# Optimization experiments

Measured on AMD Instinct MI355X. Metric: run time of the kernel, lower is better.

Reference implementation:

```python
import jax, jax.numpy as jnp
import numpy as np

D_MODEL = 256
N_HEADS = 8
D_K = D_MODEL // N_HEADS
D_HID = D_MODEL // 2
LN_EPS = 1e-5


def setup_inputs() -> dict:
    key = jax.random.key(0)
    ks = jax.random.split(key, 16)
    B, ND, NT = 4, 512, 512
    s = 1.0 / np.sqrt(D_MODEL)
    inp = {
        'detections': jax.random.normal(ks[0], (B, ND, D_MODEL), jnp.float32),
        'tracks': jax.random.normal(ks[1], (B, NT, D_MODEL), jnp.float32),
        # attention projections, torch Linear convention: W [out, in], y = x W^T + b
        'w_q': jax.random.normal(ks[2], (D_MODEL, D_MODEL), jnp.float32) * s,
        'b_q': jnp.zeros((D_MODEL,), jnp.float32),
        'w_k': jax.random.normal(ks[3], (D_MODEL, D_MODEL), jnp.float32) * s,
        'b_k': jnp.zeros((D_MODEL,), jnp.float32),
        'w_v': jax.random.normal(ks[4], (D_MODEL, D_MODEL), jnp.float32) * s,
        'b_v': jnp.zeros((D_MODEL,), jnp.float32),
        'w_o': jax.random.normal(ks[5], (D_MODEL, D_MODEL), jnp.float32) * s,
        'b_o': jnp.zeros((D_MODEL,), jnp.float32),
        # LayerNorm
        'ln_g': jnp.ones((D_MODEL,), jnp.float32),
        'ln_b': jnp.zeros((D_MODEL,), jnp.float32),
        # association head MLP
        'w1': jax.random.normal(ks[6], (D_HID, D_MODEL), jnp.float32) * s,
        'b1': jnp.zeros((D_HID,), jnp.float32),
        'w2': jax.random.normal(ks[7], (1, D_HID), jnp.float32) * (1.0 / np.sqrt(D_HID)),
        'b2': jnp.zeros((1,), jnp.float32),
    }
    return inp


def _forward(detections, tracks, w_q, b_q, w_k, b_k, w_v, b_v, w_o, b_o,
             ln_g, ln_b, w1, b1, w2, b2):
    B, ND, D = detections.shape
    NT = tracks.shape[1]
    # cross-attention: query=detections, key=value=tracks
    Q = (detections @ w_q.T + b_q).reshape(B, ND, N_HEADS, D_K).transpose(0, 2, 1, 3)
    K = (tracks @ w_k.T + b_k).reshape(B, NT, N_HEADS, D_K).transpose(0, 2, 1, 3)
    V = (tracks @ w_v.T + b_v).reshape(B, NT, N_HEADS, D_K).transpose(0, 2, 1, 3)
    scores = jnp.einsum('bhqd,bhkd->bhqk', Q, K) / np.sqrt(D_K)
    attn = jax.nn.softmax(scores, axis=-1)
    ctx = jnp.einsum('bhqk,bhkd->bhqd', attn, V)  # [B,H,ND,D_K]
    ctx = ctx.transpose(0, 2, 1, 3).reshape(B, ND, D)
    attended = ctx @ w_o.T + b_o
    # residual + LayerNorm (dropout = identity in eval)
    x = detections + attended
    mu = jnp.mean(x, axis=-1, keepdims=True)
    var = jnp.var(x, axis=-1, keepdims=True)
    xn = (x - mu) * jax.lax.rsqrt(var + LN_EPS) * ln_g + ln_b
    # pairwise broadcast-multiply + 2-layer MLP + sigmoid
    combined = xn[:, :, None, :] * tracks[:, None, :, :]  # [B,ND,NT,D]
    h = jax.nn.relu(jnp.einsum('bntd,hd->bnth', combined, w1) + b1)
    logits = jnp.einsum('bnth,oh->bnto', h, w2) + b2  # [B,ND,NT,1]
    return jax.nn.sigmoid(logits[..., 0])


def reference(detections, tracks, w_q, b_q, w_k, b_k, w_v, b_v, w_o, b_o,
              ln_g, ln_b, w1, b1, w2, b2):
    return _forward(detections, tracks, w_q, b_q, w_k, b_k, w_v, b_v, w_o, b_o,
                    ln_g, ln_b, w1, b1, w2, b2)
```

## Files before the change

### kernel.cpp

```cpp
#include <hip/hip_runtime.h>

typedef _Float16 half8 __attribute__((ext_vector_type(8)));
typedef _Float16 half4v __attribute__((ext_vector_type(4)));
typedef _Float16 half2v __attribute__((ext_vector_type(2)));
typedef float f32x4 __attribute__((ext_vector_type(4)));
typedef float f32x16 __attribute__((ext_vector_type(16)));

__device__ __forceinline__ half8 cvt8(const float4 a, const float4 b) {
    half8 r;
    r[0] = (_Float16)a.x; r[1] = (_Float16)a.y; r[2] = (_Float16)a.z; r[3] = (_Float16)a.w;
    r[4] = (_Float16)b.x; r[5] = (_Float16)b.y; r[6] = (_Float16)b.z; r[7] = (_Float16)b.w;
    return r;
}

__global__ __launch_bounds__(256) void qkv_kernel(
    const float* __restrict__ det, const float* __restrict__ trk,
    const float* __restrict__ wq, const float* __restrict__ wk,
    const float* __restrict__ wv, const float* __restrict__ bq,
    const float* __restrict__ bk, const float* __restrict__ bv,
    _Float16* __restrict__ Qh, _Float16* __restrict__ Kh,
    _Float16* __restrict__ vt)
{
    int z = blockIdx.z;
    const float* A    = (z == 0) ? det : trk;
    const float* Bm   = (z == 0) ? wq : (z == 1) ? wk : wv;
    const float* bias = (z == 0) ? bq : (z == 1) ? bk : bv;

    __shared__ _Float16 As[64][40];
    __shared__ _Float16 Bs[64][40];

    int tid = threadIdx.x, l = tid & 63, w = tid >> 6;
    int wm = (w >> 1) * 32, wn = (w & 1) * 32;
    int m0 = blockIdx.x * 64, n0 = blockIdx.y * 64;
    int lr = tid >> 2, lc = (tid & 3) * 8;
    int ko = (l >> 4) * 8, l15 = l & 15;

    f32x4 acc[2][2]{};

    for (int k0 = 0; k0 < 256; k0 += 32) {
        float4 a0 = *(const float4*)(A + (long)(m0 + lr) * 256 + k0 + lc);
        float4 a1 = *(const float4*)(A + (long)(m0 + lr) * 256 + k0 + lc + 4);
        float4 b0 = *(const float4*)(Bm + (long)(n0 + lr) * 256 + k0 + lc);
        float4 b1 = *(const float4*)(Bm + (long)(n0 + lr) * 256 + k0 + lc + 4);
        __syncthreads();
        *(half8*)&As[lr][lc] = cvt8(a0, a1);
        *(half8*)&Bs[lr][lc] = cvt8(b0, b1);
        __syncthreads();
        half8 af0 = *(const half8*)(&As[wm + l15][ko]);
        half8 af1 = *(const half8*)(&As[wm + 16 + l15][ko]);
        half8 bf0 = *(const half8*)(&Bs[wn + l15][ko]);
        half8 bf1 = *(const half8*)(&Bs[wn + 16 + l15][ko]);
        acc[0][0] = __builtin_amdgcn_mfma_f32_16x16x32_f16(af0, bf0, acc[0][0], 0, 0, 0);
        acc[0][1] = __builtin_amdgcn_mfma_f32_16x16x32_f16(af0, bf1, acc[0][1], 0, 0, 0);
        acc[1][0] = __builtin_amdgcn_mfma_f32_16x16x32_f16(af1, bf0, acc[1][0], 0, 0, 0);
        acc[1][1] = __builtin_amdgcn_mfma_f32_16x16x32_f16(af1, bf1, acc[1][1], 0, 0, 0);
    }

    #pragma unroll
    for (int mm = 0; mm < 2; ++mm)
    #pragma unroll
    for (int nn = 0; nn < 2; ++nn) {
        int row  = wm + mm * 16 + (l >> 4) * 4;
        int colg = n0 + wn + nn * 16 + l15;
        float bc = bias[colg];
        if (z == 2) {
            half4v hv;
            #pragma unroll
            for (int i = 0; i < 4; ++i) hv[i] = (_Float16)(acc[mm][nn][i] + bc);
            int grow = m0 + row;
            int bb = grow >> 9, t = grow & 511;
            long off = ((long)(bb * 8 + (colg >> 5)) * 32 + (colg & 31)) * 512 + t;
            *(half4v*)(vt + off) = hv;
        } else {
            _Float16* C = (z == 0) ? Qh : Kh;
            #pragma unroll
            for (int i = 0; i < 4; ++i)
                C[(long)(m0 + row + i) * 256 + colg] = (_Float16)(acc[mm][nn][i] + bc);
        }
    }
}

__global__ __launch_bounds__(256) void flash_kernel(
    const _Float16* __restrict__ Q, const _Float16* __restrict__ K,
    const _Float16* __restrict__ vt, _Float16* __restrict__ ctx)
{
    __shared__ _Float16 P[4][16][264];
    int bh = blockIdx.y, b = bh >> 3, h = bh & 7;
    int q0 = blockIdx.x * 64;
    int tid = threadIdx.x, l = tid & 63, w = tid >> 6;
    int l15 = l & 15, g = l >> 4;

    const _Float16* qp = Q + ((long)b * 512 + q0 + w * 16 + l15) * 256 + h * 32 + g * 8;
    half8 qf = *(const half8*)qp;
    #pragma unroll
    for (int i = 0; i < 8; ++i) qf[i] = qf[i] * (_Float16)0.17677669529663687f;

    const _Float16* kp = K + ((long)b * 512 + l15) * 256 + h * 32 + g * 8;
    const _Float16* vp = vt + ((long)bh * 32 + l15) * 512 + g * 8;

    f32x4 c0{}, c1{};
    float m_run = -3e38f, sum_run = 0.f;
    f32x4 zero{};

    #pragma unroll
    for (int hf = 0; hf < 2; ++hf) {
        f32x4 s[16];
        #pragma unroll
        for (int t = 0; t < 16; ++t) {
            half8 kf = *(const half8*)(kp + (long)(hf * 16 + t) * (16 * 256));
            s[t] = __builtin_amdgcn_mfma_f32_16x16x32_f16(kf, qf, zero, 0, 0, 0);
        }
        float m0 = -3e38f, m1 = -3e38f, m2 = -3e38f, m3 = -3e38f;
        #pragma unroll
        for (int t = 0; t < 16; ++t) {
            m0 = fmaxf(m0, s[t][0]); m1 = fmaxf(m1, s[t][1]);
            m2 = fmaxf(m2, s[t][2]); m3 = fmaxf(m3, s[t][3]);
        }
        float ml = fmaxf(fmaxf(m0, m1), fmaxf(m2, m3));
        ml = fmaxf(ml, __shfl_xor(ml, 16, 64));
        ml = fmaxf(ml, __shfl_xor(ml, 32, 64));
        float m_new = fmaxf(m_run, ml);
        float scale = __expf(m_run - m_new);
        #pragma unroll
        for (int i = 0; i < 4; ++i) { c0[i] *= scale; c1[i] *= scale; }
        sum_run *= scale;
        float s0 = 0.f, s1 = 0.f, s2 = 0.f, s3 = 0.f;
        #pragma unroll
        for (int t = 0; t < 16; ++t) {
            s[t][0] = __expf(s[t][0] - m_new); s0 += s[t][0];
            s[t][1] = __expf(s[t][1] - m_new); s1 += s[t][1];
            s[t][2] = __expf(s[t][2] - m_new); s2 += s[t][2];
            s[t][3] = __expf(s[t][3] - m_new); s3 += s[t][3];
        }
        sum_run += (s0 + s1) + (s2 + s3);
        m_run = m_new;

        #pragma unroll
        for (int t = 0; t < 16; ++t) {
            half2v p01, p23;
            p01[0] = (_Float16)s[t][0]; p01[1] = (_Float16)s[t][1];
            p23[0] = (_Float16)s[t][2]; p23[1] = (_Float16)s[t][3];
            *(half2v*)&P[w][l15][t * 16 + g * 4]     = p01;
            *(half2v*)&P[w][l15][t * 16 + g * 4 + 2] = p23;
        }
        #pragma unroll
        for (int s2i = 0; s2i < 8; ++s2i) {
            half8 bf = *(const half8*)&P[w][l15][s2i * 32 + g * 8];
            half8 a0 = *(const half8*)(vp + hf * 256 + s2i * 32);
            half8 a1 = *(const half8*)(vp + 16 * 512 + hf * 256 + s2i * 32);
            c0 = __builtin_amdgcn_mfma_f32_16x16x32_f16(a0, bf, c0, 0, 0, 0);
            c1 = __builtin_amdgcn_mfma_f32_16x16x32_f16(a1, bf, c1, 0, 0, 0);
        }
    }
    sum_run += __shfl_xor(sum_run, 16, 64);
    sum_run += __shfl_xor(sum_run, 32, 64);
    float rs = 1.f / sum_run;
    _Float16* cp = ctx + ((long)b * 512 + q0 + w * 16 + l15) * 256 + h * 32;
    #pragma unroll
    for (int i = 0; i < 4; ++i) {
        cp[g * 4 + i]      = (_Float16)(c0[i] * rs);
        cp[16 + g * 4 + i] = (_Float16)(c1[i] * rs);
    }
}

__global__ __launch_bounds__(256) void outln_kernel(
    const _Float16* __restrict__ ctx, const float* __restrict__ wo,
    const float* __restrict__ bo, const float* __restrict__ det,
    const float* __restrict__ lng, const float* __restrict__ lnb,
    _Float16* __restrict__ xn)
{
    __shared__ _Float16 As[64][40];
    __shared__ _Float16 Bs[256][40];
    __shared__ float redS[4][64], redQ[4][64], mu[64], rsv[64];

    int tid = threadIdx.x, l = tid & 63, w = tid >> 6;
    int m0 = blockIdx.x * 64;
    int wn = w * 64;
    int lr = tid >> 2, lc = (tid & 3) * 8;
    int ko = (l >> 4) * 8, l15 = l & 15, g4 = l >> 4;

    f32x4 acc[4][4]{};

    for (int k0 = 0; k0 < 256; k0 += 32) {
        half8 av = *(const half8*)(ctx + (long)(m0 + lr) * 256 + k0 + lc);
        float4 f[8];
        #pragma unroll
        for (int i = 0; i < 8; ++i)
            f[i] = *(const float4*)(wo + (long)tid * 256 + k0 + i * 4);
        __syncthreads();
        *(half8*)&As[lr][lc] = av;
        #pragma unroll
        for (int i = 0; i < 4; ++i)
            *(half8*)&Bs[tid][i * 8] = cvt8(f[2 * i], f[2 * i + 1]);
        __syncthreads();
        half8 afr[4], bfr[4];
        #pragma unroll
        for (int mm = 0; mm < 4; ++mm) afr[mm] = *(const half8*)&As[mm * 16 + l15][ko];
        #pragma unroll
        for (int nn = 0; nn < 4; ++nn) bfr[nn] = *(const half8*)&Bs[wn + nn * 16 + l15][ko];
        #pragma unroll
        for (int mm = 0; mm < 4; ++mm)
            #pragma unroll
            for (int nn = 0; nn < 4; ++nn)
                acc[mm][nn] = __builtin_amdgcn_mfma_f32_16x16x32_f16(afr[mm], bfr[nn], acc[mm][nn], 0, 0, 0);
    }

    float bov[4], gv[4], bev[4];
    #pragma unroll
    for (int nn = 0; nn < 4; ++nn) {
        int c = wn + nn * 16 + l15;
        bov[nn] = bo[c]; gv[nn] = lng[c]; bev[nn] = lnb[c];
    }
    #pragma unroll
    for (int mm = 0; mm < 4; ++mm)
    #pragma unroll
    for (int i = 0; i < 4; ++i) {
        int r = mm * 16 + g4 * 4 + i;
        float s = 0.f, q = 0.f;
        #pragma unroll
        for (int nn = 0; nn < 4; ++nn) {
            float x = acc[mm][nn][i] + bov[nn]
                    + det[(long)(m0 + r) * 256 + wn + nn * 16 + l15];
            acc[mm][nn][i] = x;
            s += x; q += x * x;
        }
        #pragma unroll
        for (int off = 1; off < 16; off <<= 1) {
            s += __shfl_xor(s, off, 64);
            q += __shfl_xor(q, off, 64);
        }
        if (l15 == 0) { redS[w][r] = s; redQ[w][r] = q; }
    }
    __syncthreads();
    if (tid < 64) {
        float S = redS[0][tid] + redS[1][tid] + redS[2][tid] + redS[3][tid];
        float Qs = redQ[0][tid] + redQ[1][tid] + redQ[2][tid] + redQ[3][tid];
        float mean = S * (1.f / 256.f);
        float var = Qs * (1.f / 256.f) - mean * mean;
        mu[tid] = mean;
        rsv[tid] = rsqrtf(var + 1e-5f);
    }
    __syncthreads();
    #pragma unroll
    for (int mm = 0; mm < 4; ++mm)
    #pragma unroll
    for (int i = 0; i < 4; ++i) {
        int r = mm * 16 + g4 * 4 + i;
        float mr = mu[r], rr = rsv[r];
        #pragma unroll
        for (int nn = 0; nn < 4; ++nn)
            xn[(long)(m0 + r) * 256 + wn + nn * 16 + l15] =
                (_Float16)((acc[mm][nn][i] - mr) * rr * gv[nn] + bev[nn]);
    }
}

__global__ __launch_bounds__(256) void mlp_kernel(
    const _Float16* __restrict__ xn, const float* __restrict__ trk,
    const float* __restrict__ w1, const float* __restrict__ w2,
    const float* __restrict__ b1, const float* __restrict__ b2,
    float* __restrict__ out)
{
    int b = blockIdx.z, n0g = blockIdx.x * 32, t0 = blockIdx.y * 32;
    int tid = threadIdx.x, l = tid & 63, w = tid >> 6;
    int l31 = l & 31, hk = (l >> 5) * 8;

    __shared__ _Float16 ts[32][264];
    __shared__ float part[4][32][33];

    {
        const float* src = trk + ((long)b * 512 + t0) * 256;
        int r = tid >> 3, c0s = (tid & 7) * 32;
        float4 f[8];
        #pragma unroll
        for (int i = 0; i < 8; ++i)
            f[i] = *(const float4*)(src + (long)r * 256 + c0s + i * 4);
        #pragma unroll
        for (int i = 0; i < 4; ++i)
            *(half8*)&ts[r][c0s + i * 8] = cvt8(f[2 * i], f[2 * i + 1]);
    }

    half8 wf[16];
    {
        const float* wp = w1 + (long)(w * 32 + l31) * 256 + hk;
        #pragma unroll
        for (int ks = 0; ks < 16; ++ks) {
            float4 fa = *(const float4*)(wp + ks * 16);
            float4 fb = *(const float4*)(wp + ks * 16 + 4);
            wf[ks] = cvt8(fa, fb);
        }
    }
    half8 bx[16];
    {
        const _Float16* xb = xn + ((long)b * 512 + n0g + l31) * 256 + hk;
        #pragma unroll
        for (int ks = 0; ks < 16; ++ks)
            bx[ks] = *(const half8*)(xb + ks * 16);
    }
    f32x16 binit, w2v;
    #pragma unroll
    for (int r = 0; r < 16; ++r) {
        int hh = w * 32 + (r & 3) + 8 * (r >> 2) + 4 * (l >> 5);
        binit[r] = b1[hh];
        w2v[r]  = w2[hh];
    }

    __syncthreads();

    for (int tl = 0; tl < 32; ++tl) {
        f32x16 acc = binit;
        #pragma unroll
        for (int ks = 0; ks < 16; ++ks) {
            half8 tf = *(const half8*)&ts[tl][ks * 16 + hk];
            half8 sa = wf[ks] * tf;
            acc = __builtin_amdgcn_mfma_f32_32x32x16_f16(sa, bx[ks], acc, 0, 0, 0);
        }
        float x = 0.f;
        #pragma unroll
        for (int r = 0; r < 16; ++r)
            x = fmaf(fmaxf(acc[r], 0.f), w2v[r], x);
        x += __shfl_xor(x, 32, 64);
        if (l < 32) part[w][tl][l] = x;
    }
    __syncthreads();

    float b2v = b2[0];
    int t = tid & 31, nbase = tid >> 5;
    float* op = out + ((long)b * 512 + n0g) * 512 + t0;
    #pragma unroll
    for (int k = 0; k < 4; ++k) {
        int nn = nbase + k * 8;
        float s = part[0][t][nn] + part[1][t][nn]
                + part[2][t][nn] + part[3][t][nn] + b2v;
        op[(long)nn * 512 + t] = 1.f / (1.f + __expf(-s));
    }
}

extern "C" void kernel_launch(void* const* d_in, const int* in_sizes, int n_in,
                              void* d_out, int out_size, void* d_ws, size_t ws_size,
                              hipStream_t stream)
{
    const float* det  = (const float*)d_in[0];
    const float* trk  = (const float*)d_in[1];
    const float* w_q  = (const float*)d_in[2];
    const float* b_q  = (const float*)d_in[3];
    const float* w_k  = (const float*)d_in[4];
    const float* b_k  = (const float*)d_in[5];
    const float* w_v  = (const float*)d_in[6];
    const float* b_v  = (const float*)d_in[7];
    const float* w_o  = (const float*)d_in[8];
    const float* b_o  = (const float*)d_in[9];
    const float* ln_g = (const float*)d_in[10];
    const float* ln_b = (const float*)d_in[11];
    const float* w1   = (const float*)d_in[12];
    const float* b1   = (const float*)d_in[13];
    const float* w2   = (const float*)d_in[14];
    const float* b2   = (const float*)d_in[15];
    float* out = (float*)d_out;

    char* ws = (char*)d_ws;
    _Float16* Q_h   = (_Float16*)(ws);
    _Float16* K_h   = (_Float16*)(ws + (size_t)1048576);
    _Float16* vt    = (_Float16*)(ws + (size_t)2097152);
    _Float16* ctx_h = (_Float16*)(ws + (size_t)3145728);
    _Float16* xn_h  = (_Float16*)(ws + (size_t)4194304);

    qkv_kernel<<<dim3(32, 4, 3), 256, 0, stream>>>(
        det, trk, w_q, w_k, w_v, b_q, b_k, b_v, Q_h, K_h, vt);
    flash_kernel<<<dim3(8, 32), 256, 0, stream>>>(Q_h, K_h, vt, ctx_h);
    outln_kernel<<<32, 256, 0, stream>>>(ctx_h, w_o, b_o, det, ln_g, ln_b, xn_h);
    mlp_kernel<<<dim3(16, 16, 4), 256, 0, stream>>>(xn_h, trk, w1, w2, b1, b2, out);

    (void)in_sizes; (void)n_in; (void)out_size; (void)ws_size;
}
```

Baseline: 208.1 us.

## Split flash keys across waves, shrink outln tiles, pre-convert MLP inputs, restructure MLP MFMAs

Flash attention now assigns 16 queries per block and splits the 512 keys across four waves, then merges their partial softmax results through shared memory, which raises the grid from 256 to 1024 blocks. Outln uses 16-row tiles and 128 blocks, and both qkv and outln prefetch the next K-slice into registers before computing. A fourth z-slice of the qkv launch converts tracks and w1 to fp16 so the MLP kernel loads half-precision data directly. The MLP inner loop switches from 32x32x16 to 16x16x32 MFMAs. The intent is better GPU occupancy and fewer redundant fp32 conversions, at the cost of an extra shared-memory merge and more workspace.

```diff
diff --git a/kernel.cpp b/kernel.cpp
--- a/kernel.cpp
+++ b/kernel.cpp
@@ -4,7 +4,6 @@
 typedef _Float16 half4v __attribute__((ext_vector_type(4)));
 typedef _Float16 half2v __attribute__((ext_vector_type(2)));
 typedef float f32x4 __attribute__((ext_vector_type(4)));
-typedef float f32x16 __attribute__((ext_vector_type(16)));
 
 __device__ __forceinline__ half8 cvt8(const float4 a, const float4 b) {
     half8 r;
@@ -18,10 +17,27 @@
     const float* __restrict__ wq, const float* __restrict__ wk,
     const float* __restrict__ wv, const float* __restrict__ bq,
     const float* __restrict__ bk, const float* __restrict__ bv,
+    const float* __restrict__ w1,
     _Float16* __restrict__ Qh, _Float16* __restrict__ Kh,
-    _Float16* __restrict__ vt)
+    _Float16* __restrict__ vt, _Float16* __restrict__ trk_h,
+    _Float16* __restrict__ w1_h)
 {
     int z = blockIdx.z;
+    if (z == 3) {
+        int flat = blockIdx.y * 32 + blockIdx.x;
+        int t0 = flat * 256 + threadIdx.x;
+        for (int i = t0; i < 131072; i += 32768) {
+            float4 v = ((const float4*)trk)[i];
+            half4v h; h[0]=(_Float16)v.x; h[1]=(_Float16)v.y; h[2]=(_Float16)v.z; h[3]=(_Float16)v.w;
+            *(half4v*)(trk_h + (long)i * 4) = h;
+        }
+        if (t0 < 8192) {
+            float4 v = ((const float4*)w1)[t0];
+            half4v h; h[0]=(_Float16)v.x; h[1]=(_Float16)v.y; h[2]=(_Float16)v.z; h[3]=(_Float16)v.w;
+            *(half4v*)(w1_h + (long)t0 * 4) = h;
+        }
+        return;
+    }
     const float* A    = (z == 0) ? det : trk;
     const float* Bm   = (z == 0) ? wq : (z == 1) ? wk : wv;
     const float* bias = (z == 0) ? bq : (z == 1) ? bk : bv;
@@ -37,15 +53,22 @@
 
     f32x4 acc[2][2]{};
 
+    float4 a0 = *(const float4*)(A + (long)(m0 + lr) * 256 + lc);
+    float4 a1 = *(const float4*)(A + (long)(m0 + lr) * 256 + lc + 4);
+    float4 b0 = *(const float4*)(Bm + (long)(n0 + lr) * 256 + lc);
+    float4 b1 = *(const float4*)(Bm + (long)(n0 + lr) * 256 + lc + 4);
+
     for (int k0 = 0; k0 < 256; k0 += 32) {
-        float4 a0 = *(const float4*)(A + (long)(m0 + lr) * 256 + k0 + lc);
-        float4 a1 = *(const float4*)(A + (long)(m0 + lr) * 256 + k0 + lc + 4);
-        float4 b0 = *(const float4*)(Bm + (long)(n0 + lr) * 256 + k0 + lc);
-        float4 b1 = *(const float4*)(Bm + (long)(n0 + lr) * 256 + k0 + lc + 4);
         __syncthreads();
         *(half8*)&As[lr][lc] = cvt8(a0, a1);
         *(half8*)&Bs[lr][lc] = cvt8(b0, b1);
         __syncthreads();
+        if (k0 + 32 < 256) {
+            a0 = *(const float4*)(A + (long)(m0 + lr) * 256 + k0 + 32 + lc);
+            a1 = *(const float4*)(A + (long)(m0 + lr) * 256 + k0 + 32 + lc + 4);
+            b0 = *(const float4*)(Bm + (long)(n0 + lr) * 256 + k0 + 32 + lc);
+            b1 = *(const float4*)(Bm + (long)(n0 + lr) * 256 + k0 + 32 + lc + 4);
+        }
         half8 af0 = *(const half8*)(&As[wm + l15][ko]);
         half8 af1 = *(const half8*)(&As[wm + 16 + l15][ko]);
         half8 bf0 = *(const half8*)(&Bs[wn + l15][ko]);
@@ -84,82 +107,94 @@
     const _Float16* __restrict__ Q, const _Float16* __restrict__ K,
     const _Float16* __restrict__ vt, _Float16* __restrict__ ctx)
 {
-    __shared__ _Float16 P[4][16][264];
+    __shared__ _Float16 P[4][16][136];
+    __shared__ float cbuf[4][16][33];
+    __shared__ float mbuf[4][16], sbuf[4][16];
+
     int bh = blockIdx.y, b = bh >> 3, h = bh & 7;
-    int q0 = blockIdx.x * 64;
+    int q0 = blockIdx.x * 16;
     int tid = threadIdx.x, l = tid & 63, w = tid >> 6;
     int l15 = l & 15, g = l >> 4;
 
-    const _Float16* qp = Q + ((long)b * 512 + q0 + w * 16 + l15) * 256 + h * 32 + g * 8;
+    const _Float16* qp = Q + ((long)b * 512 + q0 + l15) * 256 + h * 32 + g * 8;
     half8 qf = *(const half8*)qp;
     #pragma unroll
     for (int i = 0; i < 8; ++i) qf[i] = qf[i] * (_Float16)0.17677669529663687f;
 
-    const _Float16* kp = K + ((long)b * 512 + l15) * 256 + h * 32 + g * 8;
-    const _Float16* vp = vt + ((long)bh * 32 + l15) * 512 + g * 8;
-
+    const _Float16* kp = K + ((long)b * 512 + w * 128 + l15) * 256 + h * 32 + g * 8;
+    const _Float16* vp = vt + ((long)bh * 32 + l15) * 512 + w * 128 + g * 8;
+
+    f32x4 zero{};
+    f32x4 s[8];
+    #pragma unroll
+    for (int t = 0; t < 8; ++t) {
+        half8 kf = *(const half8*)(kp + (long)t * (16 * 256));
+        s[t] = __builtin_amdgcn_mfma_f32_16x16x32_f16(kf, qf, zero, 0, 0, 0);
+    }
+    float m0 = -3e38f, m1 = -3e38f, m2 = -3e38f, m3 = -3e38f;
+    #pragma unroll
+    for (int t = 0; t < 8; ++t) {
+        m0 = fmaxf(m0, s[t][0]); m1 = fmaxf(m1, s[t][1]);
+        m2 = fmaxf(m2, s[t][2]); m3 = fmaxf(m3, s[t][3]);
+    }
+    float m_loc = fmaxf(fmaxf(m0, m1), fmaxf(m2, m3));
+    m_loc = fmaxf(m_loc, __shfl_xor(m_loc, 16, 64));
+    m_loc = fmaxf(m_loc, __shfl_xor(m_loc, 32, 64));
+    float s0 = 0.f, s1 = 0.f, s2 = 0.f, s3 = 0.f;
+    #pragma unroll
+    for (int t = 0; t < 8; ++t) {
+        s[t][0] = __expf(s[t][0] - m_loc); s0 += s[t][0];
+        s[t][1] = __expf(s[t][1] - m_loc); s1 += s[t][1];
+        s[t][2] = __expf(s[t][2] - m_loc); s2 += s[t][2];
+        s[t][3] = __expf(s[t][3] - m_loc); s3 += s[t][3];
+    }
+    float sum_loc = (s0 + s1) + (s2 + s3);
+    sum_loc += __shfl_xor(sum_loc, 16, 64);
+    sum_loc += __shfl_xor(sum_loc, 32, 64);
+
+    #pragma unroll
+    for (int t = 0; t < 8; ++t) {
+        half2v p01, p23;
+        p01[0] = (_Float16)s[t][0]; p01[1] = (_Float16)s[t][1];
+        p23[0] = (_Float16)s[t][2]; p23[1] = (_Float16)s[t][3];
+        *(half2v*)&P[w][l15][t * 16 + g * 4]     = p01;
+        *(half2v*)&P[w][l15][t * 16 + g * 4 + 2] = p23;
+    }
     f32x4 c0{}, c1{};
-    float m_run = -3e38f, sum_run = 0.f;
-    f32x4 zero{};
-
-    #pragma unroll
-    for (int hf = 0; hf < 2; ++hf) {
-        f32x4 s[16];
-        #pragma unroll
-        for (int t = 0; t < 16; ++t) {
-            half8 kf = *(const half8*)(kp + (long)(hf * 16 + t) * (16 * 256));
-            s[t] = __builtin_amdgcn_mfma_f32_16x16x32_f16(kf, qf, zero, 0, 0, 0);
-        }
-        float m0 = -3e38f, m1 = -3e38f, m2 = -3e38f, m3 = -3e38f;
-        #pragma unroll
-        for (int t = 0; t < 16; ++t) {
-            m0 = fmaxf(m0, s[t][0]); m1 = fmaxf(m1, s[t][1]);
-            m2 = fmaxf(m2, s[t][2]); m3 = fmaxf(m3, s[t][3]);
-        }
-        float ml = fmaxf(fmaxf(m0, m1), fmaxf(m2, m3));
-        ml = fmaxf(ml, __shfl_xor(ml, 16, 64));
-        ml = fmaxf(ml, __shfl_xor(ml, 32, 64));
-        float m_new = fmaxf(m_run, ml);
-        float scale = __expf(m_run - m_new);
-        #pragma unroll
-        for (int i = 0; i < 4; ++i) { c0[i] *= scale; c1[i] *= scale; }
-        sum_run *= scale;
-        float s0 = 0.f, s1 = 0.f, s2 = 0.f, s3 = 0.f;
-        #pragma unroll
-        for (int t = 0; t < 16; ++t) {
-            s[t][0] = __expf(s[t][0] - m_new); s0 += s[t][0];
-            s[t][1] = __expf(s[t][1] - m_new); s1 += s[t][1];
-            s[t][2] = __expf(s[t][2] - m_new); s2 += s[t][2];
-            s[t][3] = __expf(s[t][3] - m_new); s3 += s[t][3];
-        }
-        sum_run += (s0 + s1) + (s2 + s3);
-        m_run = m_new;
-
-        #pragma unroll
-        for (int t = 0; t < 16; ++t) {
-            half2v p01, p23;
-            p01[0] = (_Float16)s[t][0]; p01[1] = (_Float16)s[t][1];
-            p23[0] = (_Float16)s[t][2]; p23[1] = (_Float16)s[t][3];
-            *(half2v*)&P[w][l15][t * 16 + g * 4]     = p01;
-            *(half2v*)&P[w][l15][t * 16 + g * 4 + 2] = p23;
-        }
-        #pragma unroll
-        for (int s2i = 0; s2i < 8; ++s2i) {
-            half8 bf = *(const half8*)&P[w][l15][s2i * 32 + g * 8];
-            half8 a0 = *(const half8*)(vp + hf * 256 + s2i * 32);
-            half8 a1 = *(const half8*)(vp + 16 * 512 + hf * 256 + s2i * 32);
-            c0 = __builtin_amdgcn_mfma_f32_16x16x32_f16(a0, bf, c0, 0, 0, 0);
-            c1 = __builtin_amdgcn_mfma_f32_16x16x32_f16(a1, bf, c1, 0, 0, 0);
-        }
-    }
-    sum_run += __shfl_xor(sum_run, 16, 64);
-    sum_run += __shfl_xor(sum_run, 32, 64);
-    float rs = 1.f / sum_run;
-    _Float16* cp = ctx + ((long)b * 512 + q0 + w * 16 + l15) * 256 + h * 32;
+    #pragma unroll
+    for (int s2i = 0; s2i < 4; ++s2i) {
+        half8 bf = *(const half8*)&P[w][l15][s2i * 32 + g * 8];
+        half8 a0 = *(const half8*)(vp + s2i * 32);
+        half8 a1 = *(const half8*)(vp + 16 * 512 + s2i * 32);
+        c0 = __builtin_amdgcn_mfma_f32_16x16x32_f16(a0, bf, c0, 0, 0, 0);
+        c1 = __builtin_amdgcn_mfma_f32_16x16x32_f16(a1, bf, c1, 0, 0, 0);
+    }
+    if (g == 0) { mbuf[w][l15] = m_loc; sbuf[w][l15] = sum_loc; }
     #pragma unroll
     for (int i = 0; i < 4; ++i) {
-        cp[g * 4 + i]      = (_Float16)(c0[i] * rs);
-        cp[16 + g * 4 + i] = (_Float16)(c1[i] * rs);
+        cbuf[w][l15][g * 4 + i]      = c0[i];
+        cbuf[w][l15][16 + g * 4 + i] = c1[i];
+    }
+    __syncthreads();
+    if (w == 0) {
+        float ma = fmaxf(fmaxf(mbuf[0][l15], mbuf[1][l15]),
+                         fmaxf(mbuf[2][l15], mbuf[3][l15]));
+        float e0 = __expf(mbuf[0][l15] - ma), e1 = __expf(mbuf[1][l15] - ma);
+        float e2 = __expf(mbuf[2][l15] - ma), e3 = __expf(mbuf[3][l15] - ma);
+        float den = sbuf[0][l15] * e0 + sbuf[1][l15] * e1
+                  + sbuf[2][l15] * e2 + sbuf[3][l15] * e3;
+        float rs = 1.f / den;
+        _Float16* cp = ctx + ((long)b * 512 + q0 + l15) * 256 + h * 32;
+        #pragma unroll
+        for (int i = 0; i < 4; ++i) {
+            int d0 = g * 4 + i, d1 = 16 + g * 4 + i;
+            float v0 = cbuf[0][l15][d0] * e0 + cbuf[1][l15][d0] * e1
+                     + cbuf[2][l15][d0] * e2 + cbuf[3][l15][d0] * e3;
+            float v1 = cbuf[0][l15][d1] * e0 + cbuf[1][l15][d1] * e1
+                     + cbuf[2][l15][d1] * e2 + cbuf[3][l15][d1] * e3;
+            cp[d0] = (_Float16)(v0 * rs);
+            cp[d1] = (_Float16)(v1 * rs);
+        }
     }
 }
 
@@ -169,40 +204,44 @@
     const float* __restrict__ lng, const float* __restrict__ lnb,
     _Float16* __restrict__ xn)
 {
-    __shared__ _Float16 As[64][40];
+    __shared__ _Float16 As[16][40];
     __shared__ _Float16 Bs[256][40];
-    __shared__ float redS[4][64], redQ[4][64], mu[64], rsv[64];
+    __shared__ float redS[4][16], redQ[4][16], mu[16], rsv[16];
 
     int tid = threadIdx.x, l = tid & 63, w = tid >> 6;
-    int m0 = blockIdx.x * 64;
-    int wn = w * 64;
-    int lr = tid >> 2, lc = (tid & 3) * 8;
-    int ko = (l >> 4) * 8, l15 = l & 15, g4 = l >> 4;
-
-    f32x4 acc[4][4]{};
+    int m0 = blockIdx.x * 16, wn = w * 64;
+    int ko = (l >> 4) * 8, l15 = l & 15, g = l >> 4;
+    int ar = tid >> 2, ac = (tid & 3) * 8;
+
+    f32x4 acc[4]{};
+
+    half8 av{};
+    float4 f[8];
+    if (tid < 64) av = *(const half8*)(ctx + (long)(m0 + ar) * 256 + ac);
+    #pragma unroll
+    for (int i = 0; i < 8; ++i)
+        f[i] = *(const float4*)(wo + (long)tid * 256 + i * 4);
 
     for (int k0 = 0; k0 < 256; k0 += 32) {
-        half8 av = *(const half8*)(ctx + (long)(m0 + lr) * 256 + k0 + lc);
-        float4 f[8];
-        #pragma unroll
-        for (int i = 0; i < 8; ++i)
-            f[i] = *(const float4*)(wo + (long)tid * 256 + k0 + i * 4);
         __syncthreads();
-        *(half8*)&As[lr][lc] = av;
+        if (tid < 64) *(half8*)&As[ar][ac] = av;
         #pragma unroll
         for (int i = 0; i < 4; ++i)
             *(half8*)&Bs[tid][i * 8] = cvt8(f[2 * i], f[2 * i + 1]);
         __syncthreads();
-        half8 afr[4], bfr[4];
-        #pragma unroll
-        for (int mm = 0; mm < 4; ++mm) afr[mm] = *(const half8*)&As[mm * 16 + l15][ko];
-        #pragma unroll
-        for (int nn = 0; nn < 4; ++nn) bfr[nn] = *(const half8*)&Bs[wn + nn * 16 + l15][ko];
-        #pragma unroll
-        for (int mm = 0; mm < 4; ++mm)
-            #pragma unroll
-            for (int nn = 0; nn < 4; ++nn)
-                acc[mm][nn] = __builtin_amdgcn_mfma_f32_16x16x32_f16(afr[mm], bfr[nn], acc[mm][nn], 0, 0, 0);
+        if (k0 + 32 < 256) {
+            if (tid < 64)
+                av = *(const half8*)(ctx + (long)(m0 + ar) * 256 + k0 + 32 + ac);
+            #pragma unroll
+            for (int i = 0; i < 8; ++i)
+                f[i] = *(const float4*)(wo + (long)tid * 256 + k0 + 32 + i * 4);
+        }
+        half8 af = *(const half8*)&As[l15][ko];
+        #pragma unroll
+        for (int nn = 0; nn < 4; ++nn) {
+            half8 bf = *(const half8*)&Bs[wn + nn * 16 + l15][ko];
+            acc[nn] = __builtin_amdgcn_mfma_f32_16x16x32_f16(af, bf, acc[nn], 0, 0, 0);
+        }
     }
 
     float bov[4], gv[4], bev[4];
@@ -212,16 +251,14 @@
         bov[nn] = bo[c]; gv[nn] = lng[c]; bev[nn] = lnb[c];
     }
     #pragma unroll
-    for (int mm = 0; mm < 4; ++mm)
-    #pragma unroll
     for (int i = 0; i < 4; ++i) {
-        int r = mm * 16 + g4 * 4 + i;
+        int r = g * 4 + i;
         float s = 0.f, q = 0.f;
         #pragma unroll
         for (int nn = 0; nn < 4; ++nn) {
-            float x = acc[mm][nn][i] + bov[nn]
+            float x = acc[nn][i] + bov[nn]
                     + det[(long)(m0 + r) * 256 + wn + nn * 16 + l15];
-            acc[mm][nn][i] = x;
+            acc[nn][i] = x;
             s += x; q += x * x;
         }
         #pragma unroll
@@ -232,100 +269,118 @@
         if (l15 == 0) { redS[w][r] = s; redQ[w][r] = q; }
     }
     __syncthreads();
-    if (tid < 64) {
-        float S = redS[0][tid] + redS[1][tid] + redS[2][tid] + redS[3][tid];
+    if (tid < 16) {
+        float S  = redS[0][tid] + redS[1][tid] + redS[2][tid] + redS[3][tid];
         float Qs = redQ[0][tid] + redQ[1][tid] + redQ[2][tid] + redQ[3][tid];
         float mean = S * (1.f / 256.f);
-        float var = Qs * (1.f / 256.f) - mean * mean;
+        float var  = Qs * (1.f / 256.f) - mean * mean;
         mu[tid] = mean;
         rsv[tid] = rsqrtf(var + 1e-5f);
     }
     __syncthreads();
     #pragma unroll
-    for (int mm = 0; mm < 4; ++mm)
-    #pragma unroll
     for (int i = 0; i < 4; ++i) {
-        int r = mm * 16 + g4 * 4 + i;
+        int r = g * 4 + i;
         float mr = mu[r], rr = rsv[r];
         #pragma unroll
         for (int nn = 0; nn < 4; ++nn)
             xn[(long)(m0 + r) * 256 + wn + nn * 16 + l15] =
-                (_Float16)((acc[mm][nn][i] - mr) * rr * gv[nn] + bev[nn]);
+                (_Float16)((acc[nn][i] - mr) * rr * gv[nn] + bev[nn]);
     }
 }
 
 __global__ __launch_bounds__(256) void mlp_kernel(
-    const _Float16* __restrict__ xn, const float* __restrict__ trk,
-    const float* __restrict__ w1, const float* __restrict__ w2,
+    const _Float16* __restrict__ xn, const _Float16* __restrict__ trk,
+    const _Float16* __restrict__ w1, const float* __restrict__ w2,
     const float* __restrict__ b1, const float* __restrict__ b2,
     float* __restrict__ out)
 {
-    int b = blockIdx.z, n0g = blockIdx.x * 32, t0 = blockIdx.y * 32;
-    int tid = threadIdx.x, l = tid & 63, w = tid >> 6;
-    int l31 = l & 31, hk = (l >> 5) * 8;
+    int b  = blockIdx.z;
+    int n0 = blockIdx.x * 32;
+    int t0 = blockIdx.y * 32;
+    int tid = threadIdx.x;
+    int l = tid & 63, w = tid >> 6;
+    int l15 = l & 15, g = l >> 4;
+    int ko = g * 8;
 
     __shared__ _Float16 ts[32][264];
     __shared__ float part[4][32][33];
 
     {
-        const float* src = trk + ((long)b * 512 + t0) * 256;
-        int r = tid >> 3, c0s = (tid & 7) * 32;
-        float4 f[8];
-        #pragma unroll
-        for (int i = 0; i < 8; ++i)
-            f[i] = *(const float4*)(src + (long)r * 256 + c0s + i * 4);
-        #pragma unroll
-        for (int i = 0; i < 4; ++i)
-            *(half8*)&ts[r][c0s + i * 8] = cvt8(f[2 * i], f[2 * i + 1]);
-    }
-
-    half8 wf[16];
+        const _Float16* src = trk + ((long)b * 512 + t0) * 256;
+        int r = tid >> 3, c0s = (tid & 7) * 8;
+        #pragma unroll
+        for (int c = 0; c < 256; c += 64)
+            *(half8*)(&ts[r][c + c0s]) = *(const half8*)(src + r * 256 + c + c0s);
+    }
+
+    half8 wf[2][8];
     {
-        const float* wp = w1 + (long)(w * 32 + l31) * 256 + hk;
-        #pragma unroll
-        for (int ks = 0; ks < 16; ++ks) {
-            float4 fa = *(const float4*)(wp + ks * 16);
-            float4 fb = *(const float4*)(wp + ks * 16 + 4);
-            wf[ks] = cvt8(fa, fb);
-        }
-    }
-    half8 bx[16];
+        const _Float16* w1p = w1 + (w * 32 + l15) * 256 + ko;
+        #pragma unroll
+        for (int a = 0; a < 2; ++a)
+            #pragma unroll
+            for (int ks = 0; ks < 8; ++ks)
+                wf[a][ks] = *(const half8*)(w1p + a * 16 * 256 + ks * 32);
+    }
+    f32x4 binit[2]; f32x4 w2v[2];
+    #pragma unroll
+    for (int a = 0; a < 2; ++a)
+        #pragma unroll
+        for (int i = 0; i < 4; ++i) {
+            int hh = w * 32 + a * 16 + g * 4 + i;
+            binit[a][i] = b1[hh];
+            w2v[a][i]   = w2[hh];
+        }
+
+    half8 bx[2][8];
     {
-        const _Float16* xb = xn + ((long)b * 512 + n0g + l31) * 256 + hk;
-        #pragma unroll
-        for (int ks = 0; ks < 16; ++ks)
-            bx[ks] = *(const half8*)(xb + ks * 16);
-    }
-    f32x16 binit, w2v;
-    #pragma unroll
-    for (int r = 0; r < 16; ++r) {
-        int hh = w * 32 + (r & 3) + 8 * (r >> 2) + 4 * (l >> 5);
-        binit[r] = b1[hh];
-        w2v[r]  = w2[hh];
+        const _Float16* xb = xn + ((long)b * 512 + n0 + l15) * 256 + ko;
+        #pragma unroll
+        for (int mm = 0; mm < 2; ++mm)
+            #pragma unroll
+            for (int ks = 0; ks < 8; ++ks)
+                bx[mm][ks] = *(const half8*)(xb + mm * 16 * 256 + ks * 32);
     }
 
     __syncthreads();
 
     for (int tl = 0; tl < 32; ++tl) {
-        f32x16 acc = binit;
-        #pragma unroll
-        for (int ks = 0; ks < 16; ++ks) {
-            half8 tf = *(const half8*)&ts[tl][ks * 16 + hk];
-            half8 sa = wf[ks] * tf;
-            acc = __builtin_amdgcn_mfma_f32_32x32x16_f16(sa, bx[ks], acc, 0, 0, 0);
-        }
-        float x = 0.f;
-        #pragma unroll
-        for (int r = 0; r < 16; ++r)
-            x = fmaf(fmaxf(acc[r], 0.f), w2v[r], x);
-        x += __shfl_xor(x, 32, 64);
-        if (l < 32) part[w][tl][l] = x;
+        f32x4 acc[2][2];
+        #pragma unroll
+        for (int a = 0; a < 2; ++a) {
+            acc[a][0] = binit[a];
+            acc[a][1] = binit[a];
+        }
+        #pragma unroll
+        for (int ks = 0; ks < 8; ++ks) {
+            half8 tf = *(const half8*)(&ts[tl][ks * 32 + ko]);
+            half8 sa0 = wf[0][ks] * tf;
+            half8 sa1 = wf[1][ks] * tf;
+            acc[0][0] = __builtin_amdgcn_mfma_f32_16x16x32_f16(sa0, bx[0][ks], acc[0][0], 0, 0, 0);
+            acc[0][1] = __builtin_amdgcn_mfma_f32_16x16x32_f16(sa0, bx[1][ks], acc[0][1], 0, 0, 0);
+            acc[1][0] = __builtin_amdgcn_mfma_f32_16x16x32_f16(sa1, bx[0][ks], acc[1][0], 0, 0, 0);
+            acc[1][1] = __builtin_amdgcn_mfma_f32_16x16x32_f16(sa1, bx[1][ks], acc[1][1], 0, 0, 0);
+        }
+        #pragma unroll
+        for (int mm = 0; mm < 2; ++mm) {
+            float x = 0.f;
+            #pragma unroll
+            for (int a = 0; a < 2; ++a)
+                #pragma unroll
+                for (int i = 0; i < 4; ++i)
+                    x = fmaf(fmaxf(acc[a][mm][i], 0.f), w2v[a][i], x);
+            x += __shfl_xor(x, 16, 64);
+            x += __shfl_xor(x, 32, 64);
+            if (g == 0) part[w][tl][mm * 16 + l15] = x;
+        }
     }
     __syncthreads();
 
     float b2v = b2[0];
-    int t = tid & 31, nbase = tid >> 5;
-    float* op = out + ((long)b * 512 + n0g) * 512 + t0;
+    int t = tid & 31;
+    int nbase = tid >> 5;
+    float* op = out + ((long)b * 512 + n0) * 512 + t0;
     #pragma unroll
     for (int k = 0; k < 4; ++k) {
         int nn = nbase + k * 8;
@@ -363,12 +418,14 @@
     _Float16* vt    = (_Float16*)(ws + (size_t)2097152);
     _Float16* ctx_h = (_Float16*)(ws + (size_t)3145728);
     _Float16* xn_h  = (_Float16*)(ws + (size_t)4194304);
-
-    qkv_kernel<<<dim3(32, 4, 3), 256, 0, stream>>>(
-        det, trk, w_q, w_k, w_v, b_q, b_k, b_v, Q_h, K_h, vt);
-    flash_kernel<<<dim3(8, 32), 256, 0, stream>>>(Q_h, K_h, vt, ctx_h);
-    outln_kernel<<<32, 256, 0, stream>>>(ctx_h, w_o, b_o, det, ln_g, ln_b, xn_h);
-    mlp_kernel<<<dim3(16, 16, 4), 256, 0, stream>>>(xn_h, trk, w1, w2, b1, b2, out);
+    _Float16* trk_h = (_Float16*)(ws + (size_t)5242880);
+    _Float16* w1_h  = (_Float16*)(ws + (size_t)6291456);
+
+    qkv_kernel<<<dim3(32, 4, 4), 256, 0, stream>>>(
+        det, trk, w_q, w_k, w_v, b_q, b_k, b_v, w1, Q_h, K_h, vt, trk_h, w1_h);
+    flash_kernel<<<dim3(32, 32), 256, 0, stream>>>(Q_h, K_h, vt, ctx_h);
+    outln_kernel<<<128, 256, 0, stream>>>(ctx_h, w_o, b_o, det, ln_g, ln_b, xn_h);
+    mlp_kernel<<<dim3(16, 16, 4), 256, 0, stream>>>(xn_h, trk_h, w1_h, w2, b1, b2, out);
 
     (void)in_sizes; (void)n_in; (void)out_size; (void)ws_size;
 }
```

Result: faster. 189.1 us (-9.1%).
